# Optimization experiments

Measured on AMD Instinct MI355X. Metric: run time of the kernel, lower is better.

The kernel has to match this reference:

```python
import jax, jax.numpy as jnp
import numpy as np

K = 3        # prediction_steps
SKIP = 1     # skip_step (forward default)
NEG = 64     # opt.negative_samples
EPS = 1e-11  # ExpNLLLoss epsilon


def setup_inputs() -> dict:
    key = jax.random.key(0)
    ks = jax.random.split(key, 8)
    B, C, H, W = 64, 256, 14, 14
    z = jax.random.normal(ks[0], (B, C, H, W), jnp.float32)
    c = jax.random.normal(ks[1], (B, C, H, W), jnp.float32)
    Wk = jax.random.normal(ks[2], (K, C, C), jnp.float32) / np.sqrt(C).astype(np.float32)
    inp = {"z": z, "c": c, "Wk": Wk}
    for k in range(1, K + 1):
        Hp = H - (k + SKIP)
        rows = Hp * W * B
        inp[f"neg_idx_k{k}"] = jax.random.randint(ks[2 + k], (rows * NEG,), 0, rows, dtype=jnp.int32)
    return inp


def _loss_k(z, c, Wk, neg_idx, k):
    # z, c: [B,C,H,W]; Wk: [Co,Ci] (1x1 conv); neg_idx: [(H-k-SKIP)*W*B*NEG]
    B, C, H, W = z.shape
    Hp = H - (k + SKIP)
    zt = z[:, :, k + SKIP:, :]                            # [B,Ci,Hp,W]
    ztwk = jnp.einsum('oc,bchw->hwbo', Wk, zt)            # [Hp,W,B,Co] (1x1 conv + permute(2,3,0,1))
    flat = ztwk.reshape(Hp * W * B, -1)
    shuf = flat[neg_idx].reshape(Hp, W, B, NEG, -1)       # gathered negatives [Hp,W,B,N,Co]
    ctx = jnp.transpose(c[:, :, :Hp, :], (2, 3, 0, 1))    # context c[:,:,:-(k+SKIP),:] -> [Hp,W,B,Co]
    main = jnp.einsum('hwbc,hwbc->hwb', ctx, ztwk)[..., None]   # [Hp,W,B,1]
    negs = jnp.einsum('hwbc,hwbnc->hwbn', ctx, shuf)            # [Hp,W,B,N]
    log_fk = jnp.concatenate([main, negs], axis=-1)             # [Hp,W,B,1+N]
    log_fk = jnp.transpose(log_fk, (2, 3, 0, 1))                # [B,1+N,Hp,W]
    probs = jax.nn.softmax(log_fk, axis=1)
    # ExpNLLLoss, target class 0, reduction='mean'
    return -jnp.mean(jnp.log(probs[:, 0] + EPS))


def reference(z, c, Wk, neg_idx_k1, neg_idx_k2, neg_idx_k3):
    idxs = [neg_idx_k1, neg_idx_k2, neg_idx_k3]
    total = 0.0
    for k in range(1, K + 1):
        total = total + _loss_k(z, c, Wk[k - 1], idxs[k - 1], k)
    return total / K
```

## Files before the change

kernel.cpp:

```cpp
#include <hip/hip_runtime.h>
#include <math.h>


typedef short bf16x8 __attribute__((ext_vector_type(8)));
typedef float f32x4 __attribute__((ext_vector_type(4)));

static __device__ __forceinline__ unsigned short f2bf(float f) {
    union { float f; unsigned int u; } x; x.f = f;
    unsigned int r = x.u + 0x7fffu + ((x.u >> 16) & 1u);
    return (unsigned short)(r >> 16);
}

static __device__ __forceinline__ unsigned char f2e4m3(float f) {
    union { float f; unsigned int u; } x; x.f = f;
    unsigned int s = (x.u >> 24) & 0x80u;
    float af = fabsf(f);
    if (af > 448.f) af = 448.f;
    x.f = af;
    unsigned int u = x.u;
    int e = (int)(u >> 23) - 127;
    unsigned int out;
    if (af == 0.f) {
        out = 0u;
    } else if (e < -6) {
        int mq = (int)rintf(af * 512.f);
        out = (mq >= 8) ? 0x08u : (unsigned int)mq;
    } else {
        unsigned int r = u + 0x7FFFFu + ((u >> 20) & 1u);
        int e2 = (int)(r >> 23) - 127;
        if (e2 > 8) out = 0x7Eu;
        else out = (unsigned int)(((e2 + 7) << 3) | ((r >> 20) & 7u));
    }
    return (unsigned char)(s | out);
}

static __device__ __forceinline__ void gload_lds4(const void* g, void* l) {
    __builtin_amdgcn_global_load_lds(
        (const __attribute__((address_space(1))) void*)g,
        (__attribute__((address_space(3))) void*)l, 4, 0, 0);
}
static __device__ __forceinline__ void gload_lds16(const void* g, void* l) {
    __builtin_amdgcn_global_load_lds(
        (const __attribute__((address_space(1))) void*)g,
        (__attribute__((address_space(3))) void*)l, 16, 0, 0);
}

__global__ __launch_bounds__(256)
void prep_kernel(const float* __restrict__ z, const float* __restrict__ c,
                 const float* __restrict__ Wk,
                 unsigned short* __restrict__ zt, unsigned char* __restrict__ ct8,
                 unsigned short* __restrict__ wkb, float* __restrict__ out) {
    __shared__ float tile[16][201];
    const int tid = threadIdx.x;
    int x = blockIdx.x;
    if (x < 768) {
        int i = x * 256 + tid;
        wkb[i] = f2bf(Wk[i]);
        if (x == 0 && tid == 0) out[0] = 0.f;
        return;
    }
    const bool isz = x < 1792;
    const int local = isz ? (x - 768) : (x - 1792);
    const float* src = isz ? z : c;
    const int b  = local & 63;
    const int c0 = (local >> 6) << 4;
    for (int i = tid; i < 16 * 196; i += 256) {
        int cc = i / 196;
        int hw = i - cc * 196;
        tile[cc][hw] = src[(size_t)((b << 8) + c0 + cc) * 196 + hw];
    }
    __syncthreads();
    if (isz) {
        for (int i = tid; i < 196 * 16; i += 256) {
            int hw = i >> 4, cc = i & 15;
            zt[(size_t)((hw << 6) + b) * 256 + c0 + cc] = f2bf(tile[cc][hw]);
        }
    } else {
        for (int i = tid; i < 196 * 16; i += 256) {
            int hw = i >> 4, cc = i & 15;
            ct8[(size_t)((hw << 6) + b) * 256 + c0 + cc] = f2e4m3(tile[cc][hw]);
        }
    }
}

#define PSTR 528
__global__ __launch_bounds__(256)
void proj_mfma_kernel(const unsigned short* __restrict__ zt,
                      const unsigned short* __restrict__ wkb,
                      unsigned char* __restrict__ ztwk) {
    __shared__ __align__(16) unsigned char smem[(64 + 32) * PSTR];
    unsigned char* smA = smem;
    unsigned char* smB = smem + 64 * PSTR;

    int x = blockIdx.y;
    int k, hw;
    if (x < 168)      { k = 0; hw = x; }
    else if (x < 322) { k = 1; hw = x - 168; }
    else              { k = 2; hw = x - 322; }
    const int o0 = blockIdx.x << 5;
    const int row0  = hw << 6;
    const int zrow0 = row0 + (((k + 2) * 14) << 6);
    unsigned char* zo = ztwk + (size_t)k * 10752 * 256;

    const int tid = threadIdx.x;
    const unsigned char* zsrc = (const unsigned char*)(zt + (size_t)zrow0 * 256);
    const unsigned char* bsrc = (const unsigned char*)(wkb + ((size_t)k << 16) + o0 * 256);

    #pragma unroll
    for (int i = 0; i < 8; ++i) {
        int sb = ((i << 8) + tid) << 4;
        int r = sb >> 9, off = sb & 511;
        *(int4*)(smA + r * PSTR + off) = *(const int4*)(zsrc + sb);
    }
    #pragma unroll
    for (int i = 0; i < 4; ++i) {
        int sb = ((i << 8) + tid) << 4;
        int r = sb >> 9, off = sb & 511;
        *(int4*)(smB + r * PSTR + off) = *(const int4*)(bsrc + sb);
    }
    __syncthreads();

    const int wv = tid >> 6, lane = tid & 63;
    const int m = lane & 15, kq = lane >> 4;
    f32x4 acc[2] = {};
    const unsigned short* aP  = (const unsigned short*)(smA + (size_t)((wv << 4) + m) * PSTR) + (kq << 3);
    const unsigned short* bP0 = (const unsigned short*)(smB + (size_t)m * PSTR) + (kq << 3);
    const unsigned short* bP1 = (const unsigned short*)(smB + (size_t)(16 + m) * PSTR) + (kq << 3);
    #pragma unroll
    for (int kk = 0; kk < 256; kk += 32) {
        bf16x8 af = *(const bf16x8*)(aP  + kk);
        bf16x8 b0 = *(const bf16x8*)(bP0 + kk);
        bf16x8 b1 = *(const bf16x8*)(bP1 + kk);
        acc[0] = __builtin_amdgcn_mfma_f32_16x16x32_bf16(af, b0, acc[0], 0, 0, 0);
        acc[1] = __builtin_amdgcn_mfma_f32_16x16x32_bf16(af, b1, acc[1], 0, 0, 0);
    }
    __syncthreads();
    unsigned char* cs = smA;
    #pragma unroll
    for (int nt = 0; nt < 2; ++nt)
        #pragma unroll
        for (int r = 0; r < 4; ++r)
            cs[(size_t)((wv << 4) + (kq << 2) + r) * 40 + (nt << 4) + m] =
                f2e4m3(acc[nt][r]);
    __syncthreads();
    {
        int r = tid >> 2, off = (tid & 3) << 3;
        unsigned long long v = *(const unsigned long long*)(cs + (size_t)r * 40 + off);
        *(unsigned long long*)(zo + (size_t)(row0 + r) * 256 + o0 + off) = v;
    }
}

__global__ __launch_bounds__(128, 4)
void loss_mfma_kernel(const unsigned char* __restrict__ ct8,
                      const unsigned char* __restrict__ ztwk8,
                      const int* __restrict__ n0, const int* __restrict__ n1,
                      const int* __restrict__ n2, float* __restrict__ rowloss) {
    __shared__ __align__(16) unsigned char slab[68 * 256];
    __shared__ __align__(16) unsigned char ctx_s[256];
    __shared__ float sred[2][2];
    const int tid = threadIdx.x;
    const int wv = tid >> 6, lane = tid & 63;
    const int m = lane & 15, kq = lane >> 4;

    int x = blockIdx.x;
    int k; const int* nb_base;
    if (x < 10752)      { k = 0; nb_base = n0; }
    else if (x < 20608) { k = 1; nb_base = n1; x -= 10752; }
    else                { k = 2; nb_base = n2; x -= 20608; }
    const int row = x;
    const unsigned char* flat8 = ztwk8 + (size_t)k * 10752 * 256;
    const float wk = (k == 0) ? (1.f / (3.f * 10752.f))
                   : (k == 1) ? (1.f / (3.f * 9856.f))
                              : (1.f / (3.f * 8960.f));
    const int rbase = (k == 0) ? 0 : (k == 1) ? 10752 : 20608;

    const int myidx = nb_base[((size_t)row << 6) + lane];
    const int lg = lane >> 4;
    const int d  = (lane & 15) << 4;

    if (wv == 0) {
        #pragma unroll
        for (int j = 0; j < 9; ++j) {
            int slot = (j << 2) + lg;
            int sel = slot - 1; if (sel < 0) sel = 0;
            int srow = __shfl(myidx, sel);
            if (slot == 0) srow = row;
            gload_lds16(flat8 + (size_t)srow * 256 + (d ^ ((slot & 7) << 4)),
                        slab + (j << 10));
        }
    } else {
        gload_lds4(ct8 + (size_t)row * 256 + (lane << 2), ctx_s);
        #pragma unroll
        for (int j = 9; j < 17; ++j) {
            int slot = (j << 2) + lg;
            int sc = slot > 64 ? 64 : slot;
            int srow = __shfl(myidx, sc - 1);
            gload_lds16(flat8 + (size_t)srow * 256 + (d ^ ((sc & 7) << 4)),
                        slab + (j << 10));
        }
    }
    __syncthreads();

    f32x4 acc[3] = {};
    const int mt0 = (wv == 0) ? 0 : 3;
    int soff[3];
    #pragma unroll
    for (int t = 0; t < 3; ++t) {
        int slot = ((mt0 + t) << 4) + m;
        if (slot > 64) slot = 64;
        soff[t] = (slot << 8) + ((kq << 3) ^ ((slot & 7) << 4));
    }
    const unsigned char* cp = ctx_s + (kq << 3);
    #pragma unroll
    for (int kk = 0; kk < 8; ++kk) {
        long long bfrag = *(const long long*)(cp + (kk << 5));
        #pragma unroll
        for (int t = 0; t < 3; ++t) {
            if (t < 2 || wv == 0) {
                long long af = *(const long long*)(slab + (soff[t] ^ (kk << 5)));
                acc[t] = __builtin_amdgcn_mfma_f32_16x16x32_fp8_fp8(af, bfrag, acc[t], 0, 0, 0);
            }
        }
    }

    float m_l = -1e30f;
    if (wv == 0) {
        #pragma unroll
        for (int t = 0; t < 3; ++t)
            #pragma unroll
            for (int r = 0; r < 4; ++r) m_l = fmaxf(m_l, acc[t][r]);
    } else {
        #pragma unroll
        for (int r = 0; r < 4; ++r) m_l = fmaxf(m_l, acc[0][r]);
        if (kq == 0) m_l = fmaxf(m_l, acc[1][0]);
    }
    m_l = fmaxf(m_l, __shfl_xor(m_l, 16));
    m_l = fmaxf(m_l, __shfl_xor(m_l, 32));

    float s_l = 0.f;
    if (wv == 0) {
        #pragma unroll
        for (int t = 0; t < 3; ++t)
            #pragma unroll
            for (int r = 0; r < 4; ++r) s_l += __expf(acc[t][r] - m_l);
    } else {
        #pragma unroll
        for (int r = 0; r < 4; ++r) s_l += __expf(acc[0][r] - m_l);
        if (kq == 0) s_l += __expf(acc[1][0] - m_l);
    }
    s_l += __shfl_xor(s_l, 16);
    s_l += __shfl_xor(s_l, 32);

    float main_l = acc[0][0];
    if (lane == 0) { sred[wv][0] = m_l; sred[wv][1] = s_l; }
    __syncthreads();
    if (tid == 0) {
        float m0 = sred[0][0], s0 = sred[0][1];
        float m1 = sred[1][0], s1 = sred[1][1];
        float mg = fmaxf(m0, m1);
        float sg = s0 * __expf(m0 - mg) + s1 * __expf(m1 - mg);
        float p0 = __expf(main_l - mg) / sg;
        rowloss[rbase + row] = -logf(p0 + 1e-11f) * wk;
    }
}

__global__ __launch_bounds__(256)
void reduce_kernel(const float* __restrict__ rl, float* __restrict__ out) {
    float s = 0.f;
    const int stride = gridDim.x * blockDim.x;
    for (int i = blockIdx.x * blockDim.x + threadIdx.x; i < 29568; i += stride)
        s += rl[i];
    #pragma unroll
    for (int off = 32; off >= 1; off >>= 1) s += __shfl_xor(s, off);
    if ((threadIdx.x & 63) == 0) atomicAdd(out, s);
}

extern "C" void kernel_launch(void* const* d_in, const int* in_sizes, int n_in,
                              void* d_out, int out_size, void* d_ws, size_t ws_size,
                              hipStream_t stream) {
    const float* z  = (const float*)d_in[0];
    const float* c  = (const float*)d_in[1];
    const float* Wk = (const float*)d_in[2];
    const int* negs[3] = {(const int*)d_in[3], (const int*)d_in[4], (const int*)d_in[5]};
    float* out = (float*)d_out;

    char* p = (char*)d_ws;
    unsigned short* zt      = (unsigned short*)p;   p += (size_t)196 * 64 * 256 * 2;
    unsigned short* wkb     = (unsigned short*)p;   p += (size_t)3 * 65536 * 2;
    unsigned char*  ct8     = (unsigned char*)p;    p += (size_t)196 * 64 * 256;
    unsigned char*  ztwk8   = (unsigned char*)p;    p += (size_t)3 * 10752 * 256;
    float*          rowloss = (float*)p;

    prep_kernel<<<2816, 256, 0, stream>>>(z, c, Wk, zt, ct8, wkb, out);
    proj_mfma_kernel<<<dim3(8, 462), 256, 0, stream>>>(zt, wkb, ztwk8);
    loss_mfma_kernel<<<29568, 128, 0, stream>>>(ct8, ztwk8, negs[0], negs[1],
                                                negs[2], rowloss);
    reduce_kernel<<<32, 256, 0, stream>>>(rowloss, out);
}
```

Baseline: 155.7 us.

## Make loss kernel persistent with triple-buffered gather pipeline and online softmax

Replaces the one-row-per-block loss kernel with 3072 persistent single-wave blocks. Each block walks rows with a stride and streams 16-row negative tiles through a triple-buffered LDS ring, using explicit vmcnt waits, while an online softmax keeps the running max and sum. Index and context loads for the next row are prefetched during the current row, and each block writes one partial sum, so the reduce kernel shrinks to 12 blocks. The aim is to hide gather latency and remove per-block launch and sync overhead, at the cost of lower occupancy per CU and fragile hand-tuned wait counts.

Result: slower. 163.6 us (+5.1%).

```diff
diff --git a/kernel.cpp b/kernel.cpp
--- a/kernel.cpp
+++ b/kernel.cpp
@@ -4,6 +4,9 @@
 
 typedef short bf16x8 __attribute__((ext_vector_type(8)));
 typedef float f32x4 __attribute__((ext_vector_type(4)));
+
+#define VWAIT(N) asm volatile("s_waitcnt vmcnt(" #N ")" ::: "memory")
+#define SB() __builtin_amdgcn_sched_barrier(0)
 
 static __device__ __forceinline__ unsigned short f2bf(float f) {
     union { float f; unsigned int u; } x; x.f = f;
@@ -150,126 +153,232 @@
     }
 }
 
-__global__ __launch_bounds__(128, 4)
+#define NSTREAM 3072
+
+static __device__ __forceinline__ void rowmeta(int gr, int* k, int* row) {
+    if (gr < 10752)      { *k = 0; *row = gr; }
+    else if (gr < 20608) { *k = 1; *row = gr - 10752; }
+    else                 { *k = 2; *row = gr - 20608; }
+}
+
+static __device__ __forceinline__ void issue_tile(
+    unsigned char* tbuf, int t, int myidx, int grow,
+    const unsigned char* f8, int lane) {
+    const int lg = lane >> 4;
+    const int c16b = (lane & 15) << 4;
+    #pragma unroll
+    for (int q = 0; q < 4; ++q) {
+        int s = (t << 4) + (q << 2) + lg;
+        int sel = s - 1; if (sel < 0) sel = 0;
+        int srow = __shfl(myidx, sel);
+        if (s == 0) srow = grow;
+        int soff = c16b ^ (((((q & 1) << 2) + lg) & 7) << 4);
+        gload_lds16(f8 + (size_t)srow * 256 + soff, tbuf + (q << 10));
+    }
+}
+static __device__ __forceinline__ void issue_tail(
+    unsigned char* tbuf, int myidx, const unsigned char* f8, int lane) {
+    const int lg = lane >> 4;
+    const int c16b = (lane & 15) << 4;
+    int srow = __shfl(myidx, 63);
+    int soff = c16b ^ ((lg & 7) << 4);
+    gload_lds16(f8 + (size_t)srow * 256 + soff, tbuf);
+}
+
+__global__ __launch_bounds__(64)
 void loss_mfma_kernel(const unsigned char* __restrict__ ct8,
                       const unsigned char* __restrict__ ztwk8,
                       const int* __restrict__ n0, const int* __restrict__ n1,
                       const int* __restrict__ n2, float* __restrict__ rowloss) {
-    __shared__ __align__(16) unsigned char slab[68 * 256];
-    __shared__ __align__(16) unsigned char ctx_s[256];
-    __shared__ float sred[2][2];
-    const int tid = threadIdx.x;
-    const int wv = tid >> 6, lane = tid & 63;
+    __shared__ __align__(16) unsigned char tb[3][4096];
+    __shared__ __align__(16) unsigned char cx[2][256];
+    __shared__ int ib[2][64];
+
+    const int lane = threadIdx.x;
     const int m = lane & 15, kq = lane >> 4;
-
-    int x = blockIdx.x;
-    int k; const int* nb_base;
-    if (x < 10752)      { k = 0; nb_base = n0; }
-    else if (x < 20608) { k = 1; nb_base = n1; x -= 10752; }
-    else                { k = 2; nb_base = n2; x -= 20608; }
-    const int row = x;
-    const unsigned char* flat8 = ztwk8 + (size_t)k * 10752 * 256;
-    const float wk = (k == 0) ? (1.f / (3.f * 10752.f))
-                   : (k == 1) ? (1.f / (3.f * 9856.f))
-                              : (1.f / (3.f * 8960.f));
-    const int rbase = (k == 0) ? 0 : (k == 1) ? 10752 : 20608;
-
-    const int myidx = nb_base[((size_t)row << 6) + lane];
-    const int lg = lane >> 4;
-    const int d  = (lane & 15) << 4;
-
-    if (wv == 0) {
-        #pragma unroll
-        for (int j = 0; j < 9; ++j) {
-            int slot = (j << 2) + lg;
-            int sel = slot - 1; if (sel < 0) sel = 0;
-            int srow = __shfl(myidx, sel);
-            if (slot == 0) srow = row;
-            gload_lds16(flat8 + (size_t)srow * 256 + (d ^ ((slot & 7) << 4)),
-                        slab + (j << 10));
-        }
-    } else {
-        gload_lds4(ct8 + (size_t)row * 256 + (lane << 2), ctx_s);
-        #pragma unroll
-        for (int j = 9; j < 17; ++j) {
-            int slot = (j << 2) + lg;
-            int sc = slot > 64 ? 64 : slot;
-            int srow = __shfl(myidx, sc - 1);
-            gload_lds16(flat8 + (size_t)srow * 256 + (d ^ ((sc & 7) << 4)),
-                        slab + (j << 10));
-        }
-    }
-    __syncthreads();
-
-    f32x4 acc[3] = {};
-    const int mt0 = (wv == 0) ? 0 : 3;
-    int soff[3];
-    #pragma unroll
-    for (int t = 0; t < 3; ++t) {
-        int slot = ((mt0 + t) << 4) + m;
-        if (slot > 64) slot = 64;
-        soff[t] = (slot << 8) + ((kq << 3) ^ ((slot & 7) << 4));
-    }
-    const unsigned char* cp = ctx_s + (kq << 3);
-    #pragma unroll
-    for (int kk = 0; kk < 8; ++kk) {
-        long long bfrag = *(const long long*)(cp + (kk << 5));
-        #pragma unroll
-        for (int t = 0; t < 3; ++t) {
-            if (t < 2 || wv == 0) {
-                long long af = *(const long long*)(slab + (soff[t] ^ (kk << 5)));
-                acc[t] = __builtin_amdgcn_mfma_f32_16x16x32_fp8_fp8(af, bfrag, acc[t], 0, 0, 0);
-            }
-        }
-    }
-
-    float m_l = -1e30f;
-    if (wv == 0) {
-        #pragma unroll
-        for (int t = 0; t < 3; ++t)
+    const int stream = blockIdx.x;
+    const int n = (29568 - stream + NSTREAM - 1) / NSTREAM;
+
+    const int asoff = m * 256 + ((kq << 3) ^ ((m & 7) << 4));
+
+    int gr = stream;
+    int k, row; rowmeta(gr, &k, &row);
+    const unsigned char* f8 = ztwk8 + (size_t)k * 10752 * 256;
+    float wkcur = (k == 0) ? (1.f / (3.f * 10752.f))
+                : (k == 1) ? (1.f / (3.f * 9856.f))
+                           : (1.f / (3.f * 8960.f));
+
+    {
+        const int* nb = (k == 0) ? n0 : (k == 1) ? n1 : n2;
+        gload_lds4(nb + ((size_t)row << 6) + lane, ib[0]);
+    }
+    VWAIT(0); SB();
+    int myidx = ib[0][lane];
+    {
+        gload_lds4(ct8 + (size_t)row * 256 + (lane << 2), cx[0]);
+        int gr1 = gr + NSTREAM;
+        int k1, row1; rowmeta(gr1, &k1, &row1);
+        const int* nb1 = (k1 == 0) ? n0 : (k1 == 1) ? n1 : n2;
+        gload_lds4(nb1 + ((size_t)row1 << 6) + lane, ib[1]);
+        issue_tile(tb[0], 0, myidx, row, f8, lane);
+        issue_tile(tb[1], 1, myidx, row, f8, lane);
+    }
+
+    float lacc = 0.f;
+    int r0 = 0;
+    int myidx_nx = 0;
+
+    for (int i = 0; i < n; ++i) {
+        const bool last = (i == n - 1);
+        int r1 = r0 + 1; if (r1 == 3) r1 = 0;
+        int r2 = r1 + 1; if (r2 == 3) r2 = 0;
+
+        int gr1 = gr + NSTREAM;
+        int k1 = k, row1 = row;
+        const unsigned char* f81 = f8;
+        if (!last) {
+            rowmeta(gr1, &k1, &row1);
+            f81 = ztwk8 + (size_t)k1 * 10752 * 256;
+        }
+
+        long long bf[8], af[8];
+        f32x4 a;
+        float m_run, s_run, mainv;
+
+        VWAIT(4); SB();
+        {
+            const unsigned char* cpx = cx[i & 1] + (kq << 3);
             #pragma unroll
-            for (int r = 0; r < 4; ++r) m_l = fmaxf(m_l, acc[t][r]);
-    } else {
-        #pragma unroll
-        for (int r = 0; r < 4; ++r) m_l = fmaxf(m_l, acc[0][r]);
-        if (kq == 0) m_l = fmaxf(m_l, acc[1][0]);
-    }
-    m_l = fmaxf(m_l, __shfl_xor(m_l, 16));
-    m_l = fmaxf(m_l, __shfl_xor(m_l, 32));
-
-    float s_l = 0.f;
-    if (wv == 0) {
-        #pragma unroll
-        for (int t = 0; t < 3; ++t)
+            for (int kk = 0; kk < 8; ++kk) bf[kk] = *(const long long*)(cpx + (kk << 5));
             #pragma unroll
-            for (int r = 0; r < 4; ++r) s_l += __expf(acc[t][r] - m_l);
-    } else {
-        #pragma unroll
-        for (int r = 0; r < 4; ++r) s_l += __expf(acc[0][r] - m_l);
-        if (kq == 0) s_l += __expf(acc[1][0] - m_l);
-    }
-    s_l += __shfl_xor(s_l, 16);
-    s_l += __shfl_xor(s_l, 32);
-
-    float main_l = acc[0][0];
-    if (lane == 0) { sred[wv][0] = m_l; sred[wv][1] = s_l; }
-    __syncthreads();
-    if (tid == 0) {
-        float m0 = sred[0][0], s0 = sred[0][1];
-        float m1 = sred[1][0], s1 = sred[1][1];
-        float mg = fmaxf(m0, m1);
-        float sg = s0 * __expf(m0 - mg) + s1 * __expf(m1 - mg);
-        float p0 = __expf(main_l - mg) / sg;
-        rowloss[rbase + row] = -logf(p0 + 1e-11f) * wk;
-    }
+            for (int kk = 0; kk < 8; ++kk) af[kk] = *(const long long*)(tb[r0] + (asoff ^ (kk << 5)));
+        }
+        SB();
+        issue_tile(tb[r2], 2, myidx, row, f8, lane);
+        a = f32x4{0.f, 0.f, 0.f, 0.f};
+        #pragma unroll
+        for (int kk = 0; kk < 8; ++kk)
+            a = __builtin_amdgcn_mfma_f32_16x16x32_fp8_fp8(af[kk], bf[kk], a, 0, 0, 0);
+        {
+            float tm = fmaxf(fmaxf(a[0], a[1]), fmaxf(a[2], a[3]));
+            tm = fmaxf(tm, __shfl_xor(tm, 16));
+            tm = fmaxf(tm, __shfl_xor(tm, 32));
+            m_run = tm;
+            s_run = __expf(a[0] - tm) + __expf(a[1] - tm)
+                  + __expf(a[2] - tm) + __expf(a[3] - tm);
+            mainv = a[0];
+        }
+
+        VWAIT(4); SB();
+        #pragma unroll
+        for (int kk = 0; kk < 8; ++kk) af[kk] = *(const long long*)(tb[r1] + (asoff ^ (kk << 5)));
+        SB();
+        issue_tile(tb[r0], 3, myidx, row, f8, lane);
+        a = f32x4{0.f, 0.f, 0.f, 0.f};
+        #pragma unroll
+        for (int kk = 0; kk < 8; ++kk)
+            a = __builtin_amdgcn_mfma_f32_16x16x32_fp8_fp8(af[kk], bf[kk], a, 0, 0, 0);
+        {
+            float tm = fmaxf(fmaxf(a[0], a[1]), fmaxf(a[2], a[3]));
+            tm = fmaxf(tm, __shfl_xor(tm, 16));
+            tm = fmaxf(tm, __shfl_xor(tm, 32));
+            float mnew = fmaxf(m_run, tm);
+            s_run = s_run * __expf(m_run - mnew)
+                  + __expf(a[0] - mnew) + __expf(a[1] - mnew)
+                  + __expf(a[2] - mnew) + __expf(a[3] - mnew);
+            m_run = mnew;
+        }
+
+        VWAIT(4); SB();
+        #pragma unroll
+        for (int kk = 0; kk < 8; ++kk) af[kk] = *(const long long*)(tb[r2] + (asoff ^ (kk << 5)));
+        SB();
+        issue_tail(tb[r1], myidx, f8, lane);
+        a = f32x4{0.f, 0.f, 0.f, 0.f};
+        #pragma unroll
+        for (int kk = 0; kk < 8; ++kk)
+            a = __builtin_amdgcn_mfma_f32_16x16x32_fp8_fp8(af[kk], bf[kk], a, 0, 0, 0);
+        {
+            float tm = fmaxf(fmaxf(a[0], a[1]), fmaxf(a[2], a[3]));
+            tm = fmaxf(tm, __shfl_xor(tm, 16));
+            tm = fmaxf(tm, __shfl_xor(tm, 32));
+            float mnew = fmaxf(m_run, tm);
+            s_run = s_run * __expf(m_run - mnew)
+                  + __expf(a[0] - mnew) + __expf(a[1] - mnew)
+                  + __expf(a[2] - mnew) + __expf(a[3] - mnew);
+            m_run = mnew;
+        }
+
+        VWAIT(1); SB();
+        #pragma unroll
+        for (int kk = 0; kk < 8; ++kk) af[kk] = *(const long long*)(tb[r0] + (asoff ^ (kk << 5)));
+        if (!last) myidx_nx = ib[(i + 1) & 1][lane];
+        SB();
+        if (!last) {
+            gload_lds4(ct8 + (size_t)row1 * 256 + (lane << 2), cx[(i + 1) & 1]);
+            int gr2 = gr + 2 * NSTREAM;
+            int k2 = k1, row2 = row1;
+            if (gr2 < 29568) rowmeta(gr2, &k2, &row2);
+            const int* nb2 = (k2 == 0) ? n0 : (k2 == 1) ? n1 : n2;
+            gload_lds4(nb2 + ((size_t)row2 << 6) + lane, ib[i & 1]);
+            issue_tile(tb[r2], 0, myidx_nx, row1, f81, lane);
+        }
+        a = f32x4{0.f, 0.f, 0.f, 0.f};
+        #pragma unroll
+        for (int kk = 0; kk < 8; ++kk)
+            a = __builtin_amdgcn_mfma_f32_16x16x32_fp8_fp8(af[kk], bf[kk], a, 0, 0, 0);
+        {
+            float tm = fmaxf(fmaxf(a[0], a[1]), fmaxf(a[2], a[3]));
+            tm = fmaxf(tm, __shfl_xor(tm, 16));
+            tm = fmaxf(tm, __shfl_xor(tm, 32));
+            float mnew = fmaxf(m_run, tm);
+            s_run = s_run * __expf(m_run - mnew)
+                  + __expf(a[0] - mnew) + __expf(a[1] - mnew)
+                  + __expf(a[2] - mnew) + __expf(a[3] - mnew);
+            m_run = mnew;
+        }
+
+        if (last) { VWAIT(0); SB(); } else { VWAIT(6); SB(); }
+        #pragma unroll
+        for (int kk = 0; kk < 8; ++kk) af[kk] = *(const long long*)(tb[r1] + (asoff ^ (kk << 5)));
+        SB();
+        if (!last) issue_tile(tb[r0], 1, myidx_nx, row1, f81, lane);
+        a = f32x4{0.f, 0.f, 0.f, 0.f};
+        #pragma unroll
+        for (int kk = 0; kk < 8; ++kk)
+            a = __builtin_amdgcn_mfma_f32_16x16x32_fp8_fp8(af[kk], bf[kk], a, 0, 0, 0);
+        {
+            float v = (kq == 0) ? a[0] : -1e30f;
+            float tm = fmaxf(v, __shfl_xor(v, 16));
+            tm = fmaxf(tm, __shfl_xor(tm, 32));
+            float mnew = fmaxf(m_run, tm);
+            s_run = s_run * __expf(m_run - mnew)
+                  + ((kq == 0) ? __expf(a[0] - mnew) : 0.f);
+            m_run = mnew;
+        }
+
+        s_run += __shfl_xor(s_run, 16);
+        s_run += __shfl_xor(s_run, 32);
+        float mainl = __shfl(mainv, 0);
+        float p0 = __expf(mainl - m_run) / s_run;
+        lacc += -logf(p0 + 1e-11f) * wkcur;
+
+        gr = gr1;
+        if (!last) {
+            k = k1; row = row1; f8 = f81; myidx = myidx_nx;
+            wkcur = (k == 0) ? (1.f / (3.f * 10752.f))
+                  : (k == 1) ? (1.f / (3.f * 9856.f))
+                             : (1.f / (3.f * 8960.f));
+        }
+        r0 = r2;
+    }
+
+    if (lane == 0) rowloss[stream] = lacc;
 }
 
 __global__ __launch_bounds__(256)
 void reduce_kernel(const float* __restrict__ rl, float* __restrict__ out) {
-    float s = 0.f;
-    const int stride = gridDim.x * blockDim.x;
-    for (int i = blockIdx.x * blockDim.x + threadIdx.x; i < 29568; i += stride)
-        s += rl[i];
+    float s = rl[blockIdx.x * 256 + threadIdx.x];
     #pragma unroll
     for (int off = 32; off >= 1; off >>= 1) s += __shfl_xor(s, off);
     if ((threadIdx.x & 63) == 0) atomicAdd(out, s);
@@ -293,7 +402,7 @@
 
     prep_kernel<<<2816, 256, 0, stream>>>(z, c, Wk, zt, ct8, wkb, out);
     proj_mfma_kernel<<<dim3(8, 462), 256, 0, stream>>>(zt, wkb, ztwk8);
-    loss_mfma_kernel<<<29568, 128, 0, stream>>>(ct8, ztwk8, negs[0], negs[1],
-                                                negs[2], rowloss);
-    reduce_kernel<<<32, 256, 0, stream>>>(rowloss, out);
-}
+    loss_mfma_kernel<<<NSTREAM, 64, 0, stream>>>(ct8, ztwk8, negs[0], negs[1],
+                                                 negs[2], rowloss);
+    reduce_kernel<<<12, 256, 0, stream>>>(rowloss, out);
+}
```
